# Kernel optimization log

Measured on AMD Instinct MI355X. Metric: run time of the kernel, lower is better.

Reference implementation:

```python
import jax, jax.numpy as jnp
import numpy as np
from jax import lax

D_MODEL = 384
D_STATE = 16
D_CONV = 4
EXPAND = 2
D_INNER = EXPAND * D_MODEL            # 768
DT_RANK = int(np.ceil(D_INNER / 16))  # 48
B_SZ, L_SEQ = 8, 1024
LN_EPS = 1e-5


def setup_inputs() -> dict:
    key = jax.random.key(0)
    ks = jax.random.split(key, 10)
    x = jax.random.normal(ks[0], (B_SZ, L_SEQ, D_MODEL), dtype=jnp.float32)
    ln_g = jnp.ones((D_MODEL,), jnp.float32)
    ln_b = jnp.zeros((D_MODEL,), jnp.float32)
    in_proj_w = jax.random.normal(ks[1], (2 * D_INNER, D_MODEL), jnp.float32) * (D_MODEL ** -0.5)
    conv_w = jax.random.normal(ks[2], (D_INNER, 1, D_CONV), jnp.float32) * (D_CONV ** -0.5)
    conv_b = jax.random.normal(ks[3], (D_INNER,), jnp.float32) * 0.01
    x_proj_w = jax.random.normal(ks[4], (DT_RANK + 2 * D_STATE, D_INNER), jnp.float32) * (D_INNER ** -0.5)
    dt_std = DT_RANK ** -0.5
    dt_proj_w = jax.random.uniform(ks[5], (D_INNER, DT_RANK), jnp.float32, -dt_std, dt_std)
    dt_proj_b = jax.random.normal(ks[6], (D_INNER,), jnp.float32) * 0.01
    A_log = jnp.log(jnp.tile(jnp.arange(1, D_STATE + 1, dtype=jnp.float32), (D_INNER, 1)))
    D_param = jnp.ones((D_INNER,), jnp.float32)
    out_proj_w = jax.random.normal(ks[7], (D_MODEL, D_INNER), jnp.float32) * (D_INNER ** -0.5)
    return {"x": x, "ln_g": ln_g, "ln_b": ln_b, "in_proj_w": in_proj_w,
            "conv_w": conv_w, "conv_b": conv_b, "x_proj_w": x_proj_w,
            "dt_proj_w": dt_proj_w, "dt_proj_b": dt_proj_b, "A_log": A_log,
            "D_param": D_param, "out_proj_w": out_proj_w}


def _selective_scan(u, delta, A, Bm, Cm):
    # u, delta: (B,L,Din); A: (Din,N); Bm, Cm: (B,L,N)
    dA = jnp.exp(delta[..., None] * A)                 # (B,L,Din,N)
    dBu = (delta * u)[..., None] * Bm[:, :, None, :]   # (B,L,Din,N)
    dA_t = jnp.moveaxis(dA, 1, 0)                      # (L,B,Din,N)
    dBu_t = jnp.moveaxis(dBu, 1, 0)
    C_t = jnp.moveaxis(Cm, 1, 0)                       # (L,B,N)

    def step(h, inp):
        dA_s, dBu_s, c_s = inp
        h = dA_s * h + dBu_s                           # (B,Din,N)
        y = jnp.einsum('bdn,bn->bd', h, c_s)
        return h, y

    h0 = jnp.zeros((u.shape[0], u.shape[2], A.shape[1]), u.dtype)
    _, ys = lax.scan(step, h0, (dA_t, dBu_t, C_t))
    return jnp.moveaxis(ys, 0, 1)                      # (B,L,Din)


def reference(x, ln_g, ln_b, in_proj_w, conv_w, conv_b, x_proj_w,
              dt_proj_w, dt_proj_b, A_log, D_param, out_proj_w):
    residual = x
    # LayerNorm
    mu = jnp.mean(x, axis=-1, keepdims=True)
    var = jnp.var(x, axis=-1, keepdims=True)
    xn = (x - mu) * lax.rsqrt(var + LN_EPS) * ln_g + ln_b
    # in_proj and split
    xz = xn @ in_proj_w.T                              # (B,L,2*Din)
    xh, z = jnp.split(xz, 2, axis=-1)
    # causal depthwise conv1d (torch pads both sides then truncates to L)
    xc = lax.conv_general_dilated(
        jnp.moveaxis(xh, 1, 2), conv_w, (1,), [(D_CONV - 1, 0)],
        feature_group_count=D_INNER,
        dimension_numbers=('NCH', 'OIH', 'NCH')) + conv_b[None, :, None]
    u = jax.nn.silu(jnp.moveaxis(xc, 1, 2))            # (B,L,Din)
    # SSM input-dependent params
    xpo = u @ x_proj_w.T                               # (B,L,dt_rank+2N)
    dlow, Bm, Cm = jnp.split(xpo, [DT_RANK, DT_RANK + D_STATE], axis=-1)
    delta = jax.nn.softplus(dlow @ dt_proj_w.T + dt_proj_b)
    A = -jnp.exp(A_log)
    y = _selective_scan(u, delta, A, Bm, Cm)
    y = y + u * D_param
    y = y * jax.nn.silu(z)
    out = y @ out_proj_w.T
    return residual + out
```

## Files before the change

kernel.cpp:

```cpp
#include <hip/hip_runtime.h>
#include <math.h>

#define DMODEL 384
#define DIN 768
#define NST 16
#define DTR 48
#define BSZ 8
#define LSEQ 1024
#define NROWS (BSZ*LSEQ)
#define XPO_W (DTR + 2*NST)
#define CL 64
#define NC (LSEQ/CL)

typedef __attribute__((ext_vector_type(8))) short bf16x8;
typedef __attribute__((ext_vector_type(4))) float f32x4;

__device__ __forceinline__ unsigned short f2bf(float x) {
  unsigned int u = __float_as_uint(x);
  unsigned int r = u + 0x7fffu + ((u >> 16) & 1u);
  return (unsigned short)(r >> 16);
}
__device__ __forceinline__ float bf2f(unsigned short h) {
  return __uint_as_float(((unsigned int)h) << 16);
}

__device__ __forceinline__ void gll16(const void* g, void* l) {
  __builtin_amdgcn_global_load_lds(
      (const __attribute__((address_space(1))) void*)g,
      (__attribute__((address_space(3))) void*)l, 16, 0, 0);
}

__global__ __launch_bounds__(256) void ln_kernel(const float* __restrict__ x,
    const float* __restrict__ g, const float* __restrict__ b,
    unsigned short* __restrict__ xh, unsigned short* __restrict__ xl) {
  int row = blockIdx.x * 4 + (threadIdx.x >> 6);
  int lane = threadIdx.x & 63;
  const float* xr = x + (size_t)row * DMODEL;
  float v[6];
  float s = 0.f, ss = 0.f;
#pragma unroll
  for (int i = 0; i < 6; ++i) { v[i] = xr[lane + i*64]; s += v[i]; ss += v[i]*v[i]; }
#pragma unroll
  for (int off = 32; off; off >>= 1) { s += __shfl_xor(s, off); ss += __shfl_xor(ss, off); }
  float mu = s * (1.f / DMODEL);
  float var = ss * (1.f / DMODEL) - mu * mu;
  float inv = rsqrtf(var + 1e-5f);
#pragma unroll
  for (int i = 0; i < 6; ++i) {
    int c = lane + i*64;
    float o = (v[i] - mu) * inv * g[c] + b[c];
    unsigned short hv = f2bf(o);
    xh[(size_t)row*DMODEL + c] = hv;
    xl[(size_t)row*DMODEL + c] = f2bf(o - bf2f(hv));
  }
}

__device__ __forceinline__ void split_one(const float* src, int ldsrc, int R, int C,
    unsigned short* dh, unsigned short* dl, int Cpad, int i) {
  int r = i / Cpad, c = i - r * Cpad;
  float v = (r < R && c < C) ? src[(size_t)r*ldsrc + c] : 0.f;
  unsigned short hv = f2bf(v);
  dh[i] = hv;
  dl[i] = f2bf(v - bf2f(hv));
}
#define N_INW (1536*384)
#define N_XW  (128*768)
#define N_DTW (768*64)
#define N_OW  (384*768)
__global__ __launch_bounds__(256) void split_weights(
    const float* __restrict__ inw, const float* __restrict__ xw,
    const float* __restrict__ dtw, const float* __restrict__ ow,
    unsigned short* inw_h, unsigned short* inw_l,
    unsigned short* xw_h, unsigned short* xw_l,
    unsigned short* dtw_h, unsigned short* dtw_l,
    unsigned short* ow_h, unsigned short* ow_l) {
  int i = blockIdx.x * 256 + threadIdx.x;
  if (i < N_INW) { split_one(inw, 384, 1536, 384, inw_h, inw_l, 384, i); return; }
  i -= N_INW;
  if (i < N_XW)  { split_one(xw, 768, 80, 768, xw_h, xw_l, 768, i); return; }
  i -= N_XW;
  if (i < N_DTW) { split_one(dtw, 48, 768, 48, dtw_h, dtw_l, 64, i); return; }
  i -= N_DTW;
  if (i < N_OW)  { split_one(ow, 768, 384, 768, ow_h, ow_l, 768, i); return; }
}

template<int EPI>
__global__ __launch_bounds__(512, 2) void gemm4(
    const unsigned short* __restrict__ Ah, const unsigned short* __restrict__ Al, int lda,
    const unsigned short* __restrict__ Bh, const unsigned short* __restrict__ Bl, int ldb,
    float* __restrict__ C, int ldc, size_t strideS,
    const float* __restrict__ bias, const float* __restrict__ res,
    int T) {
  __shared__ unsigned short lds[3][4][4096];
  int tid = threadIdx.x;
  int lane = tid & 63, wid = tid >> 6;
  int wm = wid >> 2, wn = wid & 3;

  unsigned nwg = gridDim.x * gridDim.y;
  unsigned bid = blockIdx.y * gridDim.x + blockIdx.x;
  unsigned cpx = nwg >> 3;
  unsigned sw = (bid & 7) * cpx + (bid >> 3);
  unsigned bx = sw % gridDim.x, by = sw / gridDim.x;
  int m0 = by * 128, n0 = bx * 128;
  C += (size_t)blockIdx.z * strideS;

  int srow = tid & 127, skg = tid >> 7;
  size_t ga = (size_t)(m0 + srow) * lda + skg * 8 + (size_t)blockIdx.z * T * 32;
  size_t gb = (size_t)(n0 + srow) * ldb + skg * 8 + (size_t)blockIdx.z * T * 32;
  int dst = tid * 8;

#define STAGE(bf, ko) do { \
    gll16(Ah + ga + (ko), &lds[bf][0][dst]); \
    gll16(Al + ga + (ko), &lds[bf][1][dst]); \
    gll16(Bh + gb + (ko), &lds[bf][2][dst]); \
    gll16(Bl + gb + (ko), &lds[bf][3][dst]); \
  } while (0)

  f32x4 acc[4][2];
#pragma unroll
  for (int i = 0; i < 4; ++i)
#pragma unroll
    for (int j = 0; j < 2; ++j) acc[i][j] = (f32x4){0.f, 0.f, 0.f, 0.f};

  int kgl = lane >> 4, rl = lane & 15;
  int abase = (kgl*128 + wm*64 + rl) * 8;
  int bbase = (kgl*128 + wn*32 + rl) * 8;

  STAGE(0, 0);
  if (T > 1) STAGE(1, 32);

  int cur = 0;
  for (int t = 0; t < T; ++t) {
    if (t == T - 1) asm volatile("s_waitcnt vmcnt(0)" ::: "memory");
    else            asm volatile("s_waitcnt vmcnt(4)" ::: "memory");
    __builtin_amdgcn_s_barrier();
    if (t + 2 < T) {
      int nb = cur + 2; if (nb >= 3) nb -= 3;
      STAGE(nb, (t + 2) * 32);
    }
    bf16x8 ah[4], al[4], bh[2], bl[2];
#pragma unroll
    for (int mi = 0; mi < 4; ++mi) {
      ah[mi] = *reinterpret_cast<const bf16x8*>(&lds[cur][0][abase + mi*128]);
      al[mi] = *reinterpret_cast<const bf16x8*>(&lds[cur][1][abase + mi*128]);
    }
#pragma unroll
    for (int ni = 0; ni < 2; ++ni) {
      bh[ni] = *reinterpret_cast<const bf16x8*>(&lds[cur][2][bbase + ni*128]);
      bl[ni] = *reinterpret_cast<const bf16x8*>(&lds[cur][3][bbase + ni*128]);
    }
    __builtin_amdgcn_s_setprio(1);
#pragma unroll
    for (int mi = 0; mi < 4; ++mi)
#pragma unroll
      for (int ni = 0; ni < 2; ++ni) {
        acc[mi][ni] = __builtin_amdgcn_mfma_f32_16x16x32_bf16(ah[mi], bh[ni], acc[mi][ni], 0, 0, 0);
        acc[mi][ni] = __builtin_amdgcn_mfma_f32_16x16x32_bf16(al[mi], bh[ni], acc[mi][ni], 0, 0, 0);
        acc[mi][ni] = __builtin_amdgcn_mfma_f32_16x16x32_bf16(ah[mi], bl[ni], acc[mi][ni], 0, 0, 0);
      }
    __builtin_amdgcn_s_setprio(0);
    cur = (cur == 2) ? 0 : cur + 1;
  }
#undef STAGE

#pragma unroll
  for (int mi = 0; mi < 4; ++mi)
#pragma unroll
    for (int ni = 0; ni < 2; ++ni)
#pragma unroll
      for (int j = 0; j < 4; ++j) {
        int m = m0 + wm*64 + mi*16 + (lane>>4)*4 + j;
        int n = n0 + wn*32 + ni*16 + rl;
        float v = acc[mi][ni][j];
        if (EPI == 0) {
          C[(size_t)m*ldc + n] = v;
        } else if (EPI == 2) {
          v += bias[n];
          v = (v > 20.f) ? v : log1pf(__expf(v));
          C[(size_t)m*ldc + n] = v;
        } else if (EPI == 3) {
          C[(size_t)m*ldc + n] = v + res[(size_t)m*ldc + n];
        }
      }
}

__global__ __launch_bounds__(256) void reduce_xproj(
    const float* __restrict__ P, float* __restrict__ xpo,
    unsigned short* __restrict__ dh, unsigned short* __restrict__ dl) {
  int idx = blockIdx.x * 256 + threadIdx.x;
  int m = idx >> 7, n = idx & 127;
  float v = 0.f;
#pragma unroll
  for (int s = 0; s < 4; ++s) v += P[(size_t)s * NROWS * 128 + idx];
  if (n < XPO_W) xpo[(size_t)m * XPO_W + n] = v;
  if (n < 64) {
    unsigned short hv = f2bf(v);
    dh[(size_t)m*64 + n] = hv;
    dl[(size_t)m*64 + n] = f2bf(v - bf2f(hv));
  }
}

__global__ __launch_bounds__(256) void conv_silu_kernel(
    const float* __restrict__ xz, const float* __restrict__ w,
    const float* __restrict__ cb,
    unsigned short* __restrict__ uh, unsigned short* __restrict__ ul) {
  int r = blockIdx.x / 3;
  int d = (blockIdx.x % 3) * 256 + threadIdx.x;
  int l = r & (LSEQ - 1);
  size_t idx = (size_t)r * DIN + d;
  float acc = cb[d];
#pragma unroll
  for (int j = 0; j < 4; ++j) {
    int li = l - 3 + j;
    if (li >= 0)
      acc = fmaf(xz[(size_t)(r - l + li) * (2*DIN) + d], w[d*4 + j], acc);
  }
  float s = acc / (1.f + __expf(-acc));
  unsigned short hv = f2bf(s);
  uh[idx] = hv;
  ul[idx] = f2bf(s - bf2f(hv));
}

__global__ __launch_bounds__(256) void scan_pass1(
    const float* __restrict__ delta,
    const unsigned short* __restrict__ uh, const unsigned short* __restrict__ ul,
    const float* __restrict__ xpo, const float* __restrict__ A_log,
    float* __restrict__ carryA, float* __restrict__ carryH) {
  int d = blockIdx.x * 256 + threadIdx.x;
  int c = blockIdx.y, b = blockIdx.z;
  float A[16];
  {
    const float4* al = reinterpret_cast<const float4*>(A_log + (size_t)d * NST);
#pragma unroll
    for (int i = 0; i < 4; ++i) {
      float4 t = al[i];
      A[4*i+0] = -__expf(t.x); A[4*i+1] = -__expf(t.y);
      A[4*i+2] = -__expf(t.z); A[4*i+3] = -__expf(t.w);
    }
  }
  float h[16], ap[16];
#pragma unroll
  for (int n = 0; n < 16; ++n) { h[n] = 0.f; ap[n] = 1.f; }
  const float* dp = delta + ((size_t)b*LSEQ + c*CL) * DIN + d;
  const unsigned short* uhp = uh + ((size_t)b*LSEQ + c*CL) * DIN + d;
  const unsigned short* ulp = ul + ((size_t)b*LSEQ + c*CL) * DIN + d;
  const float* bp = xpo   + ((size_t)b*LSEQ + c*CL) * XPO_W + DTR;
  for (int l = 0; l < CL; ++l) {
    float dv = dp[(size_t)l*DIN];
    float uv = bf2f(uhp[(size_t)l*DIN]) + bf2f(ulp[(size_t)l*DIN]);
    float du = dv * uv;
    float Bv[16];
    {
      const float4* b4 = reinterpret_cast<const float4*>(bp + (size_t)l*XPO_W);
#pragma unroll
      for (int i = 0; i < 4; ++i) {
        float4 t = b4[i];
        Bv[4*i+0] = t.x; Bv[4*i+1] = t.y; Bv[4*i+2] = t.z; Bv[4*i+3] = t.w;
      }
    }
#pragma unroll
    for (int n = 0; n < 16; ++n) {
      float a = __expf(dv * A[n]);
      ap[n] *= a;
      h[n] = fmaf(a, h[n], du * Bv[n]);
    }
  }
  size_t ci = (((size_t)b*NC + c) * DIN + d) * NST;
  float4* ca = reinterpret_cast<float4*>(carryA + ci);
  float4* ch = reinterpret_cast<float4*>(carryH + ci);
#pragma unroll
  for (int i = 0; i < 4; ++i) {
    ca[i] = make_float4(ap[4*i], ap[4*i+1], ap[4*i+2], ap[4*i+3]);
    ch[i] = make_float4(h[4*i],  h[4*i+1],  h[4*i+2],  h[4*i+3]);
  }
}

__global__ __launch_bounds__(256) void scan_mid(
    const float* __restrict__ carryA, float* __restrict__ carryH) {
  int idx = blockIdx.x * 256 + threadIdx.x;
  int b = idx / (DIN*NST);
  int rem = idx - b * DIN*NST;
  float h = 0.f;
#pragma unroll
  for (int c = 0; c < NC; ++c) {
    size_t i = ((size_t)b*NC + c) * (DIN*NST) + rem;
    float a = carryA[i];
    float e = carryH[i];
    carryH[i] = h;
    h = fmaf(a, h, e);
  }
}

__global__ __launch_bounds__(256) void scan_pass2(
    const float* __restrict__ delta,
    const unsigned short* __restrict__ uh, const unsigned short* __restrict__ ul,
    const float* __restrict__ xpo, const float* __restrict__ xz,
    const float* __restrict__ A_log, const float* __restrict__ Dp,
    const float* __restrict__ carryH,
    unsigned short* __restrict__ yh, unsigned short* __restrict__ yl) {
  int d = blockIdx.x * 256 + threadIdx.x;
  int c = blockIdx.y, b = blockIdx.z;
  float A[16];
  {
    const float4* al = reinterpret_cast<const float4*>(A_log + (size_t)d * NST);
#pragma unroll
    for (int i = 0; i < 4; ++i) {
      float4 t = al[i];
      A[4*i+0] = -__expf(t.x); A[4*i+1] = -__expf(t.y);
      A[4*i+2] = -__expf(t.z); A[4*i+3] = -__expf(t.w);
    }
  }
  float h[16];
  size_t ci = (((size_t)b*NC + c) * DIN + d) * NST;
  {
    const float4* ch = reinterpret_cast<const float4*>(carryH + ci);
#pragma unroll
    for (int i = 0; i < 4; ++i) {
      float4 t = ch[i];
      h[4*i+0] = t.x; h[4*i+1] = t.y; h[4*i+2] = t.z; h[4*i+3] = t.w;
    }
  }
  float Dd = Dp[d];
  const float* dp = delta + ((size_t)b*LSEQ + c*CL) * DIN + d;
  const unsigned short* uhp = uh + ((size_t)b*LSEQ + c*CL) * DIN + d;
  const unsigned short* ulp = ul + ((size_t)b*LSEQ + c*CL) * DIN + d;
  const float* bp = xpo   + ((size_t)b*LSEQ + c*CL) * XPO_W + DTR;
  const float* zp = xz    + ((size_t)b*LSEQ + c*CL) * (2*DIN) + DIN + d;
  size_t yi0 = ((size_t)b*LSEQ + c*CL) * DIN + d;
  for (int l = 0; l < CL; ++l) {
    float dv = dp[(size_t)l*DIN];
    float uv = bf2f(uhp[(size_t)l*DIN]) + bf2f(ulp[(size_t)l*DIN]);
    float du = dv * uv;
    float Bv[16], Cv[16];
    {
      const float4* b4 = reinterpret_cast<const float4*>(bp + (size_t)l*XPO_W);
#pragma unroll
      for (int i = 0; i < 4; ++i) {
        float4 t = b4[i];
        Bv[4*i+0] = t.x; Bv[4*i+1] = t.y; Bv[4*i+2] = t.z; Bv[4*i+3] = t.w;
        float4 tc = b4[i+4];
        Cv[4*i+0] = tc.x; Cv[4*i+1] = tc.y; Cv[4*i+2] = tc.z; Cv[4*i+3] = tc.w;
      }
    }
    float p = 0.f;
#pragma unroll
    for (int n = 0; n < 16; ++n) {
      float a = __expf(dv * A[n]);
      h[n] = fmaf(a, h[n], du * Bv[n]);
      p = fmaf(h[n], Cv[n], p);
    }
    float z = zp[(size_t)l*(2*DIN)];
    float sz = z / (1.f + __expf(-z));
    float yv = fmaf(uv, Dd, p) * sz;
    unsigned short hv = f2bf(yv);
    yh[yi0 + (size_t)l*DIN] = hv;
    yl[yi0 + (size_t)l*DIN] = f2bf(yv - bf2f(hv));
  }
}

extern "C" void kernel_launch(void* const* d_in, const int* in_sizes, int n_in,
                              void* d_out, int out_size, void* d_ws, size_t ws_size,
                              hipStream_t stream) {
  const float* x          = (const float*)d_in[0];
  const float* ln_g       = (const float*)d_in[1];
  const float* ln_b       = (const float*)d_in[2];
  const float* in_proj_w  = (const float*)d_in[3];
  const float* conv_w     = (const float*)d_in[4];
  const float* conv_b     = (const float*)d_in[5];
  const float* x_proj_w   = (const float*)d_in[6];
  const float* dt_proj_w  = (const float*)d_in[7];
  const float* dt_proj_b  = (const float*)d_in[8];
  const float* A_log      = (const float*)d_in[9];
  const float* D_param    = (const float*)d_in[10];
  const float* out_proj_w = (const float*)d_in[11];

  char* w = (char*)d_ws;
  unsigned short* xn_h  = (unsigned short*)w;
  unsigned short* xn_l  = xn_h + (size_t)NROWS*DMODEL;
  unsigned short* dlow_h = (unsigned short*)w;
  unsigned short* dlow_l = dlow_h + (size_t)NROWS*64;
  float* carryA = (float*)w;
  float* carryH = carryA + (size_t)BSZ*NC*DIN*NST;
  char* p = w + (size_t)NROWS*DMODEL*4;
  float* xz = (float*)p;              p += (size_t)NROWS*2*DIN*4;
  unsigned short* u_h = (unsigned short*)p;
  unsigned short* u_l = u_h + (size_t)NROWS*DIN;      p += (size_t)NROWS*DIN*4;
  float* xpo = (float*)p;             p += (size_t)NROWS*XPO_W*4;
  float* delta = (float*)p;           p += (size_t)NROWS*DIN*4;
  unsigned short* inw_h = (unsigned short*)delta;
  unsigned short* inw_l = inw_h + (size_t)1536*384;
  unsigned short* xw_h  = inw_l + (size_t)1536*384;
  unsigned short* xw_l  = xw_h + (size_t)128*768;
  unsigned short* y2_h = (unsigned short*)p;
  unsigned short* y2_l = y2_h + (size_t)NROWS*DIN;
  float* xpart = (float*)p;           p += (size_t)NROWS*DIN*4;
  unsigned short* dtw_h = (unsigned short*)p;
  unsigned short* dtw_l = dtw_h + (size_t)768*64;
  unsigned short* ow_h  = dtw_l + (size_t)768*64;
  unsigned short* ow_l  = ow_h + (size_t)384*768;

  split_weights<<<(N_INW+N_XW+N_DTW+N_OW)/256, 256, 0, stream>>>(
      in_proj_w, x_proj_w, dt_proj_w, out_proj_w,
      inw_h, inw_l, xw_h, xw_l, dtw_h, dtw_l, ow_h, ow_l);

  ln_kernel<<<NROWS/4, 256, 0, stream>>>(x, ln_g, ln_b, xn_h, xn_l);

  gemm4<0><<<dim3(12, 64, 1), 512, 0, stream>>>(xn_h, xn_l, DMODEL, inw_h, inw_l, DMODEL,
      xz, 2*DIN, 0, nullptr, nullptr, 12);

  conv_silu_kernel<<<NROWS*3, 256, 0, stream>>>(xz, conv_w, conv_b, u_h, u_l);

  gemm4<0><<<dim3(1, 64, 4), 512, 0, stream>>>(u_h, u_l, DIN, xw_h, xw_l, DIN,
      xpart, 128, (size_t)NROWS*128, nullptr, nullptr, 6);
  reduce_xproj<<<(NROWS*128)/256, 256, 0, stream>>>(xpart, xpo, dlow_h, dlow_l);

  gemm4<2><<<dim3(6, 64, 1), 512, 0, stream>>>(dlow_h, dlow_l, 64, dtw_h, dtw_l, 64,
      delta, DIN, 0, dt_proj_b, nullptr, 2);

  {
    dim3 g1(DIN/256, NC, BSZ);
    scan_pass1<<<g1, 256, 0, stream>>>(delta, u_h, u_l, xpo, A_log, carryA, carryH);
    scan_mid<<<(BSZ*DIN*NST)/256, 256, 0, stream>>>(carryA, carryH);
    scan_pass2<<<g1, 256, 0, stream>>>(delta, u_h, u_l, xpo, xz, A_log, D_param,
                                       carryH, y2_h, y2_l);
  }

  gemm4<3><<<dim3(3, 64, 1), 512, 0, stream>>>(y2_h, y2_l, DIN, ow_h, ow_l, DIN,
      (float*)d_out, DMODEL, 0, nullptr, x, 24);
}
```

Baseline: 276.1 us.

## Rework GEMM to 4-wave 64x64 warp tiles, split-K out_proj, vectorize conv

Replaces the 8-wave GEMM, where each wave computed a 64x32 tile, with a 4-wave version where each wave computes 64x64. Buffering drops from triple to double, the next stage is issued after the LDS reads complete, and the MFMAs are regrouped by hi/lo component. The out_proj GEMM becomes a 2-way split-K that writes partials, plus a separate reduce kernel that adds the residual. The conv+SiLU kernel handles two channels per thread with float2 loads and packed 32-bit stores. Register reuse and the arithmetic-to-LDS ratio should improve, at the cost of fewer waves to hide latency, an extra barrier per k-step, and extra partial-sum traffic for out_proj.

```diff
diff --git a/kernel.cpp b/kernel.cpp
--- a/kernel.cpp
+++ b/kernel.cpp
@@ -85,16 +85,16 @@
 }
 
 template<int EPI>
-__global__ __launch_bounds__(512, 2) void gemm4(
+__global__ __launch_bounds__(256, 2) void gemm5(
     const unsigned short* __restrict__ Ah, const unsigned short* __restrict__ Al, int lda,
     const unsigned short* __restrict__ Bh, const unsigned short* __restrict__ Bl, int ldb,
     float* __restrict__ C, int ldc, size_t strideS,
     const float* __restrict__ bias, const float* __restrict__ res,
     int T) {
-  __shared__ unsigned short lds[3][4][4096];
+  __shared__ unsigned short lds[2][4][4096];
   int tid = threadIdx.x;
   int lane = tid & 63, wid = tid >> 6;
-  int wm = wid >> 2, wn = wid & 3;
+  int wm = wid >> 1, wn = wid & 1;
 
   unsigned nwg = gridDim.x * gridDim.y;
   unsigned bid = blockIdx.y * gridDim.x + blockIdx.x;
@@ -103,74 +103,89 @@
   unsigned bx = sw % gridDim.x, by = sw / gridDim.x;
   int m0 = by * 128, n0 = bx * 128;
   C += (size_t)blockIdx.z * strideS;
-
-  int srow = tid & 127, skg = tid >> 7;
-  size_t ga = (size_t)(m0 + srow) * lda + skg * 8 + (size_t)blockIdx.z * T * 32;
-  size_t gb = (size_t)(n0 + srow) * ldb + skg * 8 + (size_t)blockIdx.z * T * 32;
-  int dst = tid * 8;
+  size_t kofs = (size_t)blockIdx.z * T * 32;
+
+  int r0 = tid & 127, kg0 = tid >> 7;
+  int r1 = r0, kg1 = kg0 + 2;
+  size_t ga0 = (size_t)(m0 + r0) * lda + kg0*8 + kofs;
+  size_t ga1 = (size_t)(m0 + r1) * lda + kg1*8 + kofs;
+  size_t gb0 = (size_t)(n0 + r0) * ldb + kg0*8 + kofs;
+  size_t gb1 = (size_t)(n0 + r1) * ldb + kg1*8 + kofs;
+  int d0 = (wid*64) * 8;
+  int d1 = (256 + wid*64) * 8;
 
 #define STAGE(bf, ko) do { \
-    gll16(Ah + ga + (ko), &lds[bf][0][dst]); \
-    gll16(Al + ga + (ko), &lds[bf][1][dst]); \
-    gll16(Bh + gb + (ko), &lds[bf][2][dst]); \
-    gll16(Bl + gb + (ko), &lds[bf][3][dst]); \
+    gll16(Ah + ga0 + (ko), &lds[bf][0][d0]); \
+    gll16(Al + ga0 + (ko), &lds[bf][1][d0]); \
+    gll16(Bh + gb0 + (ko), &lds[bf][2][d0]); \
+    gll16(Bl + gb0 + (ko), &lds[bf][3][d0]); \
+    gll16(Ah + ga1 + (ko), &lds[bf][0][d1]); \
+    gll16(Al + ga1 + (ko), &lds[bf][1][d1]); \
+    gll16(Bh + gb1 + (ko), &lds[bf][2][d1]); \
+    gll16(Bl + gb1 + (ko), &lds[bf][3][d1]); \
   } while (0)
 
-  f32x4 acc[4][2];
+  f32x4 acc[4][4];
 #pragma unroll
   for (int i = 0; i < 4; ++i)
 #pragma unroll
-    for (int j = 0; j < 2; ++j) acc[i][j] = (f32x4){0.f, 0.f, 0.f, 0.f};
+    for (int j = 0; j < 4; ++j) acc[i][j] = (f32x4){0.f, 0.f, 0.f, 0.f};
 
   int kgl = lane >> 4, rl = lane & 15;
-  int abase = (kgl*128 + wm*64 + rl) * 8;
-  int bbase = (kgl*128 + wn*32 + rl) * 8;
 
   STAGE(0, 0);
   if (T > 1) STAGE(1, 32);
 
-  int cur = 0;
   for (int t = 0; t < T; ++t) {
-    if (t == T - 1) asm volatile("s_waitcnt vmcnt(0)" ::: "memory");
-    else            asm volatile("s_waitcnt vmcnt(4)" ::: "memory");
+    if (t + 1 < T) asm volatile("s_waitcnt vmcnt(8)" ::: "memory");
+    else           asm volatile("s_waitcnt vmcnt(0)" ::: "memory");
     __builtin_amdgcn_s_barrier();
-    if (t + 2 < T) {
-      int nb = cur + 2; if (nb >= 3) nb -= 3;
-      STAGE(nb, (t + 2) * 32);
-    }
-    bf16x8 ah[4], al[4], bh[2], bl[2];
+    int cur = t & 1;
+    bf16x8 ah[4], al[4], bh[4], bl[4];
 #pragma unroll
     for (int mi = 0; mi < 4; ++mi) {
-      ah[mi] = *reinterpret_cast<const bf16x8*>(&lds[cur][0][abase + mi*128]);
-      al[mi] = *reinterpret_cast<const bf16x8*>(&lds[cur][1][abase + mi*128]);
-    }
-#pragma unroll
-    for (int ni = 0; ni < 2; ++ni) {
-      bh[ni] = *reinterpret_cast<const bf16x8*>(&lds[cur][2][bbase + ni*128]);
-      bl[ni] = *reinterpret_cast<const bf16x8*>(&lds[cur][3][bbase + ni*128]);
-    }
+      int cell = kgl*128 + wm*64 + mi*16 + rl;
+      ah[mi] = *reinterpret_cast<const bf16x8*>(&lds[cur][0][cell*8]);
+      al[mi] = *reinterpret_cast<const bf16x8*>(&lds[cur][1][cell*8]);
+    }
+#pragma unroll
+    for (int ni = 0; ni < 4; ++ni) {
+      int cell = kgl*128 + wn*64 + ni*16 + rl;
+      bh[ni] = *reinterpret_cast<const bf16x8*>(&lds[cur][2][cell*8]);
+      bl[ni] = *reinterpret_cast<const bf16x8*>(&lds[cur][3][cell*8]);
+    }
+    asm volatile("s_waitcnt lgkmcnt(0)" ::: "memory");
+    __builtin_amdgcn_sched_barrier(0);
+    __builtin_amdgcn_s_barrier();
+    if (t + 2 < T) STAGE(cur, (t + 2) * 32);
     __builtin_amdgcn_s_setprio(1);
 #pragma unroll
     for (int mi = 0; mi < 4; ++mi)
 #pragma unroll
-      for (int ni = 0; ni < 2; ++ni) {
+      for (int ni = 0; ni < 4; ++ni)
         acc[mi][ni] = __builtin_amdgcn_mfma_f32_16x16x32_bf16(ah[mi], bh[ni], acc[mi][ni], 0, 0, 0);
+#pragma unroll
+    for (int mi = 0; mi < 4; ++mi)
+#pragma unroll
+      for (int ni = 0; ni < 4; ++ni)
         acc[mi][ni] = __builtin_amdgcn_mfma_f32_16x16x32_bf16(al[mi], bh[ni], acc[mi][ni], 0, 0, 0);
+#pragma unroll
+    for (int mi = 0; mi < 4; ++mi)
+#pragma unroll
+      for (int ni = 0; ni < 4; ++ni)
         acc[mi][ni] = __builtin_amdgcn_mfma_f32_16x16x32_bf16(ah[mi], bl[ni], acc[mi][ni], 0, 0, 0);
-      }
     __builtin_amdgcn_s_setprio(0);
-    cur = (cur == 2) ? 0 : cur + 1;
   }
 #undef STAGE
 
 #pragma unroll
   for (int mi = 0; mi < 4; ++mi)
 #pragma unroll
-    for (int ni = 0; ni < 2; ++ni)
+    for (int ni = 0; ni < 4; ++ni)
 #pragma unroll
       for (int j = 0; j < 4; ++j) {
         int m = m0 + wm*64 + mi*16 + (lane>>4)*4 + j;
-        int n = n0 + wn*32 + ni*16 + rl;
+        int n = n0 + wn*64 + ni*16 + rl;
         float v = acc[mi][ni][j];
         if (EPI == 0) {
           C[(size_t)m*ldc + n] = v;
@@ -200,25 +215,37 @@
   }
 }
 
+__global__ __launch_bounds__(256) void reduce_out(
+    const float* __restrict__ P, const float* __restrict__ x, float* __restrict__ out) {
+  int i = blockIdx.x * 256 + threadIdx.x;
+  out[i] = x[i] + P[i] + P[i + (size_t)NROWS*DMODEL];
+}
+
 __global__ __launch_bounds__(256) void conv_silu_kernel(
     const float* __restrict__ xz, const float* __restrict__ w,
     const float* __restrict__ cb,
-    unsigned short* __restrict__ uh, unsigned short* __restrict__ ul) {
-  int r = blockIdx.x / 3;
-  int d = (blockIdx.x % 3) * 256 + threadIdx.x;
+    unsigned int* __restrict__ uh, unsigned int* __restrict__ ul) {
+  int i = blockIdx.x * 256 + threadIdx.x;
+  int r = i / (DIN/2);
+  int d = (i - r * (DIN/2)) * 2;
   int l = r & (LSEQ - 1);
-  size_t idx = (size_t)r * DIN + d;
-  float acc = cb[d];
+  float a0 = cb[d], a1 = cb[d+1];
 #pragma unroll
   for (int j = 0; j < 4; ++j) {
     int li = l - 3 + j;
-    if (li >= 0)
-      acc = fmaf(xz[(size_t)(r - l + li) * (2*DIN) + d], w[d*4 + j], acc);
-  }
-  float s = acc / (1.f + __expf(-acc));
-  unsigned short hv = f2bf(s);
-  uh[idx] = hv;
-  ul[idx] = f2bf(s - bf2f(hv));
+    if (li >= 0) {
+      const float* src = &xz[(size_t)(r - l + li) * (2*DIN) + d];
+      float2 v = *reinterpret_cast<const float2*>(src);
+      a0 = fmaf(v.x, w[d*4 + j], a0);
+      a1 = fmaf(v.y, w[(d+1)*4 + j], a1);
+    }
+  }
+  float s0 = a0 / (1.f + __expf(-a0));
+  float s1 = a1 / (1.f + __expf(-a1));
+  unsigned short h0 = f2bf(s0), h1 = f2bf(s1);
+  unsigned short l0 = f2bf(s0 - bf2f(h0)), l1 = f2bf(s1 - bf2f(h1));
+  uh[i] = (unsigned int)h0 | ((unsigned int)h1 << 16);
+  ul[i] = (unsigned int)l0 | ((unsigned int)l1 << 16);
 }
 
 __global__ __launch_bounds__(256) void scan_pass1(
@@ -398,6 +425,7 @@
   unsigned short* dtw_l = dtw_h + (size_t)768*64;
   unsigned short* ow_h  = dtw_l + (size_t)768*64;
   unsigned short* ow_l  = ow_h + (size_t)384*768;
+  float* opart = xz;
 
   split_weights<<<(N_INW+N_XW+N_DTW+N_OW)/256, 256, 0, stream>>>(
       in_proj_w, x_proj_w, dt_proj_w, out_proj_w,
@@ -405,16 +433,17 @@
 
   ln_kernel<<<NROWS/4, 256, 0, stream>>>(x, ln_g, ln_b, xn_h, xn_l);
 
-  gemm4<0><<<dim3(12, 64, 1), 512, 0, stream>>>(xn_h, xn_l, DMODEL, inw_h, inw_l, DMODEL,
+  gemm5<0><<<dim3(12, 64, 1), 256, 0, stream>>>(xn_h, xn_l, DMODEL, inw_h, inw_l, DMODEL,
       xz, 2*DIN, 0, nullptr, nullptr, 12);
 
-  conv_silu_kernel<<<NROWS*3, 256, 0, stream>>>(xz, conv_w, conv_b, u_h, u_l);
-
-  gemm4<0><<<dim3(1, 64, 4), 512, 0, stream>>>(u_h, u_l, DIN, xw_h, xw_l, DIN,
+  conv_silu_kernel<<<(NROWS*DIN/2)/256, 256, 0, stream>>>(xz, conv_w, conv_b,
+      (unsigned int*)u_h, (unsigned int*)u_l);
+
+  gemm5<0><<<dim3(1, 64, 4), 256, 0, stream>>>(u_h, u_l, DIN, xw_h, xw_l, DIN,
       xpart, 128, (size_t)NROWS*128, nullptr, nullptr, 6);
   reduce_xproj<<<(NROWS*128)/256, 256, 0, stream>>>(xpart, xpo, dlow_h, dlow_l);
 
-  gemm4<2><<<dim3(6, 64, 1), 512, 0, stream>>>(dlow_h, dlow_l, 64, dtw_h, dtw_l, 64,
+  gemm5<2><<<dim3(6, 64, 1), 256, 0, stream>>>(dlow_h, dlow_l, 64, dtw_h, dtw_l, 64,
       delta, DIN, 0, dt_proj_b, nullptr, 2);
 
   {
@@ -425,6 +454,7 @@
                                        carryH, y2_h, y2_l);
   }
 
-  gemm4<3><<<dim3(3, 64, 1), 512, 0, stream>>>(y2_h, y2_l, DIN, ow_h, ow_l, DIN,
-      (float*)d_out, DMODEL, 0, nullptr, x, 24);
-}
+  gemm5<0><<<dim3(3, 64, 2), 256, 0, stream>>>(y2_h, y2_l, DIN, ow_h, ow_l, DIN,
+      opart, DMODEL, (size_t)NROWS*DMODEL, nullptr, nullptr, 12);
+  reduce_out<<<(NROWS*DMODEL)/256, 256, 0, stream>>>(opart, x, (float*)d_out);
+}
```

After: 301.8 us. 9.3% more time.
